# Kernel tuning notes

Measured on AMD Instinct MI355X. Metric: run time of the kernel, lower is better.

The kernel has to match this reference:

```python
import jax, jax.numpy as jnp
import numpy as np

B, T, I, H, V, E = 512, 256, 256, 1024, 1024, 8
FUT = 64


def _lstm_cell(x_t, h, c, Wih, Whh, b):
    # PyTorch gate order: i, f, g, o. b = b_ih + b_hh (mathematically identical).
    z = x_t @ Wih.T + h @ Whh.T + b  # [B, 4H]
    i, f, g, o = jnp.split(z, 4, axis=-1)
    i = jax.nn.sigmoid(i)
    f = jax.nn.sigmoid(f)
    g = jnp.tanh(g)
    o = jax.nn.sigmoid(o)
    c_new = f * c + i * g
    h_new = o * jnp.tanh(c_new)
    return h_new, c_new


def setup_inputs() -> dict:
    key = jax.random.key(0)
    ks = jax.random.split(key, 10)
    s = 0.02
    return {
        "x_hist": jax.random.normal(ks[0], (B, T, I), jnp.float32),
        "enc_Wih": jax.random.normal(ks[1], (4 * H, I), jnp.float32) * s,
        "enc_Whh": jax.random.normal(ks[2], (4 * H, H), jnp.float32) * s,
        "enc_b": jnp.zeros((4 * H,), jnp.float32),
        "embed_W": jax.random.normal(ks[3], (V, E), jnp.float32),
        "dec_Wih": jax.random.normal(ks[4], (4 * H, E), jnp.float32) * s,
        "dec_Whh": jax.random.normal(ks[5], (4 * H, H), jnp.float32) * s,
        "dec_b": jnp.zeros((4 * H,), jnp.float32),
        "fc_W": jax.random.normal(ks[6], (V, H), jnp.float32) * s,
        "fc_b": jnp.zeros((V,), jnp.float32),
        "future_len": FUT,
    }


def reference(x_hist, enc_Wih, enc_Whh, enc_b, embed_W, dec_Wih, dec_Whh,
              dec_b, fc_W, fc_b, future_len):
    bsz = x_hist.shape[0]
    h0 = jnp.zeros((bsz, enc_Whh.shape[1]), x_hist.dtype)
    c0 = jnp.zeros_like(h0)

    # Encoder LSTM over history (batch_first): scan over time.
    def enc_step(carry, x_t):
        h, c = carry
        h, c = _lstm_cell(x_t, h, c, enc_Wih, enc_Whh, enc_b)
        return (h, c), None

    (h, c), _ = jax.lax.scan(enc_step, (h0, c0), jnp.swapaxes(x_hist, 0, 1))

    y0 = jnp.zeros((bsz,), jnp.int32)

    def dec_step(carry, _):
        h, c, y_prev = carry
        x = embed_W[y_prev]                       # [B, E] embedding lookup
        h, c = _lstm_cell(x, h, c, dec_Wih, dec_Whh, dec_b)
        logits = h @ fc_W.T + fc_b                # [B, V]
        y = jnp.argmax(logits, axis=1).astype(jnp.int32)
        return (h, c, y), logits

    _, logits = jax.lax.scan(dec_step, (h, c, y0), None, length=future_len)
    return jnp.swapaxes(logits, 0, 1)             # [B, future_len, V]
```

## Files before the change

kernel.cpp:

```cpp
#include <hip/hip_runtime.h>
#include <cmath>

typedef __attribute__((ext_vector_type(8))) short short8;
typedef __attribute__((ext_vector_type(4))) float f32x4;

#define B_SZ 512
#define T_SZ 256
#define I_SZ 256
#define H_SZ 1024
#define V_SZ 1024
#define E_SZ 8
#define FUT 64

#define KVE 3840
#define KVD 3200
#define KVF 3072
#define APE 2560
#define APD 2176

static __device__ __forceinline__ ushort f2bf(float v) {
    uint32_t u = __float_as_uint(v);
    uint32_t r = (u + 0x7fffu + ((u >> 16) & 1u)) >> 16;
    return (ushort)r;
}
static __device__ __forceinline__ float bf2f(ushort b) {
    return __uint_as_float(((uint32_t)b) << 16);
}
static __device__ __forceinline__ uint32_t fmono(float f) {
    uint32_t u = __float_as_uint(f);
    return (u & 0x80000000u) ? ~u : (u | 0x80000000u);
}
template<int N>
static __device__ __forceinline__ void waitvm() {
    if constexpr (N == 0)      asm volatile("s_waitcnt vmcnt(0)" ::: "memory");
    else if constexpr (N == 2) asm volatile("s_waitcnt vmcnt(2)" ::: "memory");
    else if constexpr (N == 3) asm volatile("s_waitcnt vmcnt(3)" ::: "memory");
    else if constexpr (N == 4) asm volatile("s_waitcnt vmcnt(4)" ::: "memory");
    else if constexpr (N == 6) asm volatile("s_waitcnt vmcnt(6)" ::: "memory");
}

#define GLD16(gp, lp)                                                          \
    __builtin_amdgcn_global_load_lds(                                         \
        (const __attribute__((address_space(1))) void*)(gp),                  \
        (__attribute__((address_space(3))) void*)(lp), 16, 0, 0)

template<int MFR, int NFR, int NTPX,
         int NKP, int PT1, int PO0, int PO1,
         int NKS, int ST1, int SO0, int SO1, bool GATES>
__global__ __launch_bounds__(256) void gemm_step(
    const ushort* __restrict__ A, int astr,
    const ushort* __restrict__ W, int kv,
    const float* __restrict__ bias,
    float* __restrict__ c,
    ushort* __restrict__ hdest, int ldh,
    const float* __restrict__ xsrc, ushort* __restrict__ xdest,
    float* __restrict__ out, int ldo,
    unsigned long long* __restrict__ keys)
{
    constexpr int ABUF = MFR * 2048;
    constexpr int WBUF = NFR * 4096;
    __shared__ __align__(16) ushort lds[3 * ABUF + 3 * WBUF];

    const int tid = threadIdx.x;
    const int lane = tid & 63;
    const int wid = tid >> 6;
    const int wm = wid >> 1, wn = wid & 1;
    const int l15 = lane & 15, lq = lane >> 4;
    const int l7 = lane & 7, l3 = lane >> 3;

    const int flat = blockIdx.x;
    const int xcd = flat & 7, slot = flat >> 3;
    const int n_tile = xcd * NTPX + (slot % NTPX);
    const int m_tile = slot / NTPX;
    const int m0 = m_tile * (MFR * 32);
    const int n0 = n_tile * (NFR * 32);

    f32x4 acc[MFR][NFR];
#pragma unroll
    for (int m = 0; m < MFR; ++m)
#pragma unroll
        for (int n = 0; n < NFR; ++n) { f32x4 z = {0.f, 0.f, 0.f, 0.f}; acc[m][n] = z; }

    auto stageA = [&](int kcA, int bufi) {
        ushort* ab = &lds[bufi * ABUF];
#pragma unroll
        for (int i = 0; i < MFR; ++i) {
            const int rowg = (i * 4 + wid) * 8;
            const int row = rowg + l3;
            GLD16(A + (size_t)(m0 + row) * astr + kcA + ((l7 ^ (row & 7)) * 8),
                  ab + rowg * 64);
        }
    };
    auto stageP = [&](int p, int bufi) {
        stageA(p * 64 + (p < PT1 ? PO0 : PO1), bufi);
        const int kcW = p * 128;
        ushort* wb = &lds[3 * ABUF + bufi * WBUF];
#pragma unroll
        for (int i = 0; i < 2 * NFR; ++i) {
            const int rowg = (i * 4 + wid) * 4;
            const int row = rowg + lq;
            GLD16(W + (size_t)(n0 + row) * kv + kcW + ((l15 ^ (row & 15)) * 8),
                  wb + rowg * 128);
        }
    };
    auto stageS = [&](int s, int bufi) {
        stageA(s * 64 + (s < ST1 ? SO0 : SO1), bufi);
        const int kcW = NKP * 128 + s * 64;
        ushort* wb = &lds[3 * ABUF + bufi * WBUF];
#pragma unroll
        for (int i = 0; i < NFR; ++i) {
            const int rowg = (i * 4 + wid) * 8;
            const int row = rowg + l3;
            GLD16(W + (size_t)(n0 + row) * kv + kcW + ((l7 ^ (row & 7)) * 8),
                  wb + rowg * 64);
        }
    };
    auto compP = [&](int bufi) {
        const ushort* ab = &lds[bufi * ABUF];
        const ushort* wb = &lds[3 * ABUF + bufi * WBUF];
#pragma unroll
        for (int kk = 0; kk < 2; ++kk) {
            short8 af[MFR];
#pragma unroll
            for (int m = 0; m < MFR; ++m) {
                const int row = wm * (MFR * 16) + m * 16 + l15;
                af[m] = *(const short8*)
                    &ab[row * 64 + (((kk * 4 + lq) ^ (row & 7)) * 8)];
            }
#pragma unroll
            for (int sub = 0; sub < 2; ++sub) {
                short8 wf[NFR];
#pragma unroll
                for (int n = 0; n < NFR; ++n) {
                    const int row = wn * (NFR * 16) + n * 16 + l15;
                    wf[n] = *(const short8*)
                        &wb[row * 128 + (((sub * 8 + kk * 4 + lq) ^ (row & 15)) * 8)];
                }
#pragma unroll
                for (int m = 0; m < MFR; ++m)
#pragma unroll
                    for (int n = 0; n < NFR; ++n)
                        acc[m][n] = __builtin_amdgcn_mfma_f32_16x16x32_bf16(
                            af[m], wf[n], acc[m][n], 0, 0, 0);
            }
        }
    };
    auto compS = [&](int bufi) {
        const ushort* ab = &lds[bufi * ABUF];
        const ushort* wb = &lds[3 * ABUF + bufi * WBUF];
#pragma unroll
        for (int kk = 0; kk < 2; ++kk) {
            short8 af[MFR], wf[NFR];
#pragma unroll
            for (int m = 0; m < MFR; ++m) {
                const int row = wm * (MFR * 16) + m * 16 + l15;
                af[m] = *(const short8*)
                    &ab[row * 64 + (((kk * 4 + lq) ^ (row & 7)) * 8)];
            }
#pragma unroll
            for (int n = 0; n < NFR; ++n) {
                const int row = wn * (NFR * 16) + n * 16 + l15;
                wf[n] = *(const short8*)
                    &wb[row * 64 + (((kk * 4 + lq) ^ (row & 7)) * 8)];
            }
#pragma unroll
            for (int m = 0; m < MFR; ++m)
#pragma unroll
                for (int n = 0; n < NFR; ++n)
                    acc[m][n] = __builtin_amdgcn_mfma_f32_16x16x32_bf16(
                        af[m], wf[n], acc[m][n], 0, 0, 0);
        }
    };

    auto STG = [&](int i, int b) { if (i < NKP) stageP(i, b); else stageS(i - NKP, b); };

    constexpr int NT = NKP + NKS;
    constexpr int GP = MFR + 2 * NFR;
    constexpr int GS = MFR + NFR;

    STG(0, 0);
    STG(1, 1);
#pragma unroll 1
    for (int i0 = 0; i0 < NT; i0 += 3) {
#pragma unroll
        for (int j = 0; j < 3; ++j) {
            const int i = i0 + j;
            if (i < NT) {
                if (i + 1 < NKP)     waitvm<GP>();
                else if (i + 1 < NT) waitvm<GS>();
                else                 waitvm<0>();
                __builtin_amdgcn_s_barrier();
                if (i + 2 < NT) STG(i + 2, (j + 2) % 3);
                if (i < NKP) compP(j); else compS(j);
            }
        }
    }

    if constexpr (GATES) {
        float* zs = (float*)&lds[0];
        __syncthreads();
#pragma unroll
        for (int m = 0; m < MFR; ++m)
#pragma unroll
            for (int n = 0; n < NFR; ++n)
#pragma unroll
                for (int r = 0; r < 4; ++r)
                    zs[(wm * 32 + m * 16 + lq * 4 + r) * 65 +
                       wn * 32 + n * 16 + l15] = acc[m][n][r];
        __syncthreads();

        const int row = tid & 63;
        const int jl0 = (tid >> 6) * 4;
        const int grow = m0 + row;
        const int jg = n_tile * 16 + jl0;
        const f32x4 bi4 = *(const f32x4*)&bias[n0 + jl0];
        const f32x4 bf4 = *(const f32x4*)&bias[n0 + 16 + jl0];
        const f32x4 bg4 = *(const f32x4*)&bias[n0 + 32 + jl0];
        const f32x4 bo4 = *(const f32x4*)&bias[n0 + 48 + jl0];
        f32x4 cv = *(f32x4*)&c[(size_t)grow * H_SZ + jg];
        ushort hh[4], hl[4];
#pragma unroll
        for (int jj = 0; jj < 4; ++jj) {
            const float zi = zs[row * 65 + jl0 + jj] + bi4[jj];
            const float zf = zs[row * 65 + 16 + jl0 + jj] + bf4[jj];
            const float zg = zs[row * 65 + 32 + jl0 + jj] + bg4[jj];
            const float zo = zs[row * 65 + 48 + jl0 + jj] + bo4[jj];
            const float ig = 1.f / (1.f + expf(-zi));
            const float fg = 1.f / (1.f + expf(-zf));
            const float gg = tanhf(zg);
            const float og = 1.f / (1.f + expf(-zo));
            const float cn = fg * cv[jj] + ig * gg;
            cv[jj] = cn;
            const float hv = og * tanhf(cn);
            hh[jj] = f2bf(hv);
            hl[jj] = f2bf(hv - bf2f(hh[jj]));
        }
        *(f32x4*)&c[(size_t)grow * H_SZ + jg] = cv;
        ushort* hd = hdest + (size_t)grow * ldh + jg;
        uint hv2[2], lv2[2];
        hv2[0] = (uint)hh[0] | ((uint)hh[1] << 16);
        hv2[1] = (uint)hh[2] | ((uint)hh[3] << 16);
        lv2[0] = (uint)hl[0] | ((uint)hl[1] << 16);
        lv2[1] = (uint)hl[2] | ((uint)hl[3] << 16);
        *(uint*)&hd[0] = hv2[0];
        *(uint*)&hd[2] = hv2[1];
        *(uint*)&hd[1024] = lv2[0];
        *(uint*)&hd[1026] = lv2[1];

        if (xdest) {
            const int idx = flat * 256 + tid;
            const int b = idx >> 8, i = idx & 255;
            const float v = xsrc[(size_t)b * (T_SZ * I_SZ) + i];
            const ushort hi = f2bf(v), lo = f2bf(v - bf2f(hi));
            xdest[(size_t)b * APE + i] = hi;
            xdest[(size_t)b * APE + 256 + i] = lo;
        }
    } else {
        float vals[4];
        const int col = n0 + wn * 16 + l15;
        const float bv = bias[col];
#pragma unroll
        for (int r = 0; r < 4; ++r) {
            const int row = m0 + wm * 16 + lq * 4 + r;
            vals[r] = acc[0][0][r] + bv;
            out[(size_t)row * ldo + col] = vals[r];
        }
        if (keys) {
            float* zs = (float*)&lds[0];
            __syncthreads();
#pragma unroll
            for (int r = 0; r < 4; ++r)
                zs[(wm * 16 + lq * 4 + r) * 33 + wn * 16 + l15] = vals[r];
            __syncthreads();
            if (tid < 32) {
                const int row = tid;
                float best = zs[row * 33];
                int bc = 0;
#pragma unroll
                for (int cc = 1; cc < 32; ++cc) {
                    const float x = zs[row * 33 + cc];
                    if (x > best) { best = x; bc = cc; }
                }
                const unsigned long long key =
                    ((unsigned long long)fmono(best) << 32) |
                    (unsigned long long)(V_SZ - 1 - (n0 + bc));
                atomicMax(&keys[m0 + row], key);
            }
        }
    }
}

__global__ __launch_bounds__(256) void gather_embed(
    unsigned long long* __restrict__ keys,
    const float* __restrict__ embed_W,
    ushort* __restrict__ xdest)
{
    const int idx = blockIdx.x * 256 + threadIdx.x;
    const int b = idx >> 3, e = idx & 7;
    const unsigned long long key = keys[b];
    const int yb = V_SZ - 1 - (int)(key & 0xffffffffu);
    const float v = embed_W[(size_t)yb * E_SZ + e];
    const ushort hi = f2bf(v), lo = f2bf(v - bf2f(hi));
    ushort* xd = xdest + (size_t)b * APD;
    xd[e] = hi;
    xd[8 + e] = hi;
    xd[16 + e] = lo;
    if (e == 0) keys[b] = 0ull;
}

__global__ void pack_enc(const float* __restrict__ Wih, const float* __restrict__ Whh,
                         const float* __restrict__ b, ushort* __restrict__ Wp,
                         float* __restrict__ bp)
{
    const int k = blockIdx.x * 256 + threadIdx.x;
    const int np = blockIdx.y;
    const int orig = ((np >> 4) & 3) * H_SZ + (np >> 6) * 16 + (np & 15);
    float v; bool lo = false;
    if (k < 2560) {
        const int p = k >> 7, cc = k & 63;
        lo = (k >> 6) & 1;
        v = (p < 4) ? Wih[(size_t)orig * I_SZ + p * 64 + cc]
                    : Whh[(size_t)orig * H_SZ + (p - 4) * 64 + cc];
    } else {
        const int s = (k - 2560) >> 6, cc = k & 63;
        v = (s < 4) ? Wih[(size_t)orig * I_SZ + s * 64 + cc]
                    : Whh[(size_t)orig * H_SZ + (s - 4) * 64 + cc];
    }
    const ushort hi = f2bf(v);
    Wp[(size_t)np * KVE + k] = lo ? f2bf(v - bf2f(hi)) : hi;
    if (k == 0) bp[np] = b[orig];
}

__global__ void pack_dec(const float* __restrict__ Wih, const float* __restrict__ Whh,
                         const float* __restrict__ b, ushort* __restrict__ Wp,
                         float* __restrict__ bp)
{
    const int k = blockIdx.x * 256 + threadIdx.x;
    const int np = blockIdx.y;
    if (k >= KVD) return;
    const int orig = ((np >> 4) & 3) * H_SZ + (np >> 6) * 16 + (np & 15);
    float v = 0.f; bool lo = false; bool zero = false;
    if (k < 2048) {
        const int p = k >> 7, cc = k & 63;
        lo = (k >> 6) & 1;
        v = Whh[(size_t)orig * H_SZ + p * 64 + cc];
    } else {
        const int s = (k - 2048) >> 6, cc = k & 63;
        if (s < 2) {
            const int j = s * 64 + cc;
            if (j < 8)       v = Wih[(size_t)orig * E_SZ + j];
            else if (j < 16) { v = Wih[(size_t)orig * E_SZ + j - 8]; lo = true; }
            else if (j < 24) v = Wih[(size_t)orig * E_SZ + j - 16];
            else             zero = true;
        } else {
            v = Whh[(size_t)orig * H_SZ + (s - 2) * 64 + cc];
        }
    }
    ushort w = 0;
    if (!zero) { const ushort hi = f2bf(v); w = lo ? f2bf(v - bf2f(hi)) : hi; }
    Wp[(size_t)np * KVD + k] = w;
    if (k == 0) bp[np] = b[orig];
}

__global__ void pack_fc(const float* __restrict__ W, ushort* __restrict__ Wp)
{
    const int k = blockIdx.x * 256 + threadIdx.x;
    const int np = blockIdx.y;
    float v; bool lo = false;
    if (k < 2048) {
        const int p = k >> 7, cc = k & 63;
        lo = (k >> 6) & 1;
        v = W[(size_t)np * H_SZ + p * 64 + cc];
    } else {
        const int s = (k - 2048) >> 6, cc = k & 63;
        v = W[(size_t)np * H_SZ + s * 64 + cc];
    }
    const ushort hi = f2bf(v);
    Wp[(size_t)np * KVF + k] = lo ? f2bf(v - bf2f(hi)) : hi;
}

__global__ void init_all(const float* __restrict__ x0,
                         const float* __restrict__ embed_W,
                         float* __restrict__ c,
                         ushort* __restrict__ Aenc0,
                         ushort* __restrict__ Adec0,
                         ushort* __restrict__ Adec1,
                         unsigned long long* __restrict__ keys)
{
    const int idx = blockIdx.x * 256 + threadIdx.x;
    {
        const int b = idx >> 11, k = idx & 2047;
        Aenc0[(size_t)b * APE + 512 + k] = 0;
    }
    if (idx < B_SZ * H_SZ) c[idx] = 0.f;
    if (idx < B_SZ) keys[idx] = 0ull;
    if (idx < B_SZ * I_SZ) {
        const int b = idx >> 8, i = idx & 255;
        const float v = x0[(size_t)b * (T_SZ * I_SZ) + i];
        const ushort hi = f2bf(v), lo = f2bf(v - bf2f(hi));
        Aenc0[(size_t)b * APE + i] = hi;
        Aenc0[(size_t)b * APE + 256 + i] = lo;
    }
    if (idx < B_SZ * 104) {
        const int b = idx / 104, col = 24 + idx % 104;
        Adec0[(size_t)b * APD + col] = 0;
        Adec1[(size_t)b * APD + col] = 0;
    }
    if (idx < B_SZ * 24) {
        const int b = idx / 24, col = idx % 24;
        float v;
        if (col < 8)       v = embed_W[col];
        else if (col < 16) v = embed_W[col - 8];
        else               v = embed_W[col - 16];
        const ushort hi = f2bf(v);
        Adec0[(size_t)b * APD + col] = (col < 16) ? hi : f2bf(v - bf2f(hi));
    }
}

extern "C" void kernel_launch(void* const* d_in, const int* in_sizes, int n_in,
                              void* d_out, int out_size, void* d_ws, size_t ws_size,
                              hipStream_t stream)
{
    const float* x_hist  = (const float*)d_in[0];
    const float* enc_Wih = (const float*)d_in[1];
    const float* enc_Whh = (const float*)d_in[2];
    const float* enc_b   = (const float*)d_in[3];
    const float* embed_W = (const float*)d_in[4];
    const float* dec_Wih = (const float*)d_in[5];
    const float* dec_Whh = (const float*)d_in[6];
    const float* dec_b   = (const float*)d_in[7];
    const float* fc_W    = (const float*)d_in[8];
    const float* fc_b    = (const float*)d_in[9];
    float* out = (float*)d_out;

    char* p = (char*)d_ws;
    auto alloc = [&](size_t bytes) {
        char* r = p;
        p += (bytes + 255) & ~(size_t)255;
        return r;
    };
    ushort* W_enc  = (ushort*)alloc((size_t)4096 * KVE * 2);
    ushort* W_dec  = (ushort*)alloc((size_t)4096 * KVD * 2);
    ushort* W_fc   = (ushort*)alloc((size_t)1024 * KVF * 2);
    ushort* A_enc0 = (ushort*)alloc((size_t)B_SZ * APE * 2);
    ushort* A_enc1 = (ushort*)alloc((size_t)B_SZ * APE * 2);
    ushort* A_dec0 = (ushort*)alloc((size_t)B_SZ * APD * 2);
    ushort* A_dec1 = (ushort*)alloc((size_t)B_SZ * APD * 2);
    float*  cbuf   = (float*)alloc((size_t)B_SZ * H_SZ * 4);
    float*  bpe    = (float*)alloc(4096 * 4);
    float*  bpd    = (float*)alloc(4096 * 4);
    unsigned long long* keys = (unsigned long long*)alloc(B_SZ * 8);

    const dim3 blk(256);
    hipLaunchKernelGGL(pack_enc, dim3(15, 4096), blk, 0, stream, enc_Wih, enc_Whh, enc_b, W_enc, bpe);
    hipLaunchKernelGGL(pack_dec, dim3(13, 4096), blk, 0, stream, dec_Wih, dec_Whh, dec_b, W_dec, bpd);
    hipLaunchKernelGGL(pack_fc,  dim3(12, 1024), blk, 0, stream, fc_W, W_fc);
    hipLaunchKernelGGL(init_all, dim3(4096), blk, 0, stream, x_hist, embed_W, cbuf, A_enc0, A_dec0, A_dec1, keys);

    ushort* Ae[2] = {A_enc0, A_enc1};
    ushort* Ad[2] = {A_dec0, A_dec1};

    for (int t = 0; t < T_SZ; ++t) {
        ushort* hdst; int ldh; const float* xs; ushort* xd;
        if (t < T_SZ - 1) {
            hdst = Ae[(t + 1) & 1] + 512; ldh = APE;
            xs = x_hist + (size_t)(t + 1) * I_SZ;
            xd = Ae[(t + 1) & 1];
        } else {
            hdst = Ad[0] + 128; ldh = APD;
            xs = nullptr; xd = nullptr;
        }
        hipLaunchKernelGGL((gemm_step<2, 2, 8, 20, 4, 0, 256, 20, 4, 256, 1280, true>),
                           dim3(512), blk, 0, stream,
                           Ae[t & 1], APE, W_enc, KVE, bpe, cbuf,
                           hdst, ldh, xs, xd, (float*)nullptr, 0,
                           (unsigned long long*)nullptr);
    }

    for (int t = 0; t < FUT; ++t) {
        hipLaunchKernelGGL((gemm_step<2, 2, 8, 16, 16, 128, 128, 18, 2, 0, 1024, true>),
                           dim3(512), blk, 0, stream,
                           Ad[t & 1], APD, W_dec, KVD, bpd, cbuf,
                           Ad[(t + 1) & 1] + 128, APD,
                           (const float*)nullptr, (ushort*)nullptr,
                           (float*)nullptr, 0,
                           (unsigned long long*)nullptr);
        float* logits = out + (size_t)t * V_SZ;
        hipLaunchKernelGGL((gemm_step<1, 1, 4, 16, 16, 128, 128, 16, 16, 1152, 1152, false>),
                           dim3(512), blk, 0, stream,
                           Ad[(t + 1) & 1], APD, W_fc, KVF, fc_b,
                           (float*)nullptr, (ushort*)nullptr, 0,
                           (const float*)nullptr, (ushort*)nullptr,
                           logits, FUT * V_SZ, keys);
        hipLaunchKernelGGL(gather_embed, dim3(16), blk, 0, stream,
                           keys, embed_W, Ad[(t + 1) & 1]);
    }
}
```

Baseline: 9.829 ms.

## Store activations in MFMA fragment-tiled layout and load A directly to registers

Activation matrices (x, h hi/lo, embeddings) are now written in a fragment-native tiled layout of 16-row by 32-column tiles, so each lane can load its MFMA A operand straight from global memory into registers. This removes A staging through LDS and the LDS reads that fed it, which shrinks shared memory to weight buffers only. All producers (the gates epilogue, init_all, gather_embed) are rewritten to scatter into the new layout. In exchange, A fragments are held in registers across a three-deep prefetch ring, which raises register pressure, and the direct global loads may coalesce less well than the previous LDS path.

```diff
diff --git a/kernel.cpp b/kernel.cpp
--- a/kernel.cpp
+++ b/kernel.cpp
@@ -37,6 +37,7 @@
     else if constexpr (N == 3) asm volatile("s_waitcnt vmcnt(3)" ::: "memory");
     else if constexpr (N == 4) asm volatile("s_waitcnt vmcnt(4)" ::: "memory");
     else if constexpr (N == 6) asm volatile("s_waitcnt vmcnt(6)" ::: "memory");
+    else if constexpr (N == 8) asm volatile("s_waitcnt vmcnt(8)" ::: "memory");
 }
 
 #define GLD16(gp, lp)                                                          \
@@ -52,14 +53,13 @@
     const ushort* __restrict__ W, int kv,
     const float* __restrict__ bias,
     float* __restrict__ c,
-    ushort* __restrict__ hdest, int ldh,
+    ushort* __restrict__ hdest, int hoff, int hkt,
     const float* __restrict__ xsrc, ushort* __restrict__ xdest,
     float* __restrict__ out, int ldo,
     unsigned long long* __restrict__ keys)
 {
-    constexpr int ABUF = MFR * 2048;
     constexpr int WBUF = NFR * 4096;
-    __shared__ __align__(16) ushort lds[3 * ABUF + 3 * WBUF];
+    __shared__ __align__(16) ushort lds[3 * WBUF];
 
     const int tid = threadIdx.x;
     const int lane = tid & 63;
@@ -74,6 +74,7 @@
     const int m_tile = slot / NTPX;
     const int m0 = m_tile * (MFR * 32);
     const int n0 = n_tile * (NFR * 32);
+    const int KT = astr >> 5;
 
     f32x4 acc[MFR][NFR];
 #pragma unroll
@@ -81,20 +82,9 @@
 #pragma unroll
         for (int n = 0; n < NFR; ++n) { f32x4 z = {0.f, 0.f, 0.f, 0.f}; acc[m][n] = z; }
 
-    auto stageA = [&](int kcA, int bufi) {
-        ushort* ab = &lds[bufi * ABUF];
-#pragma unroll
-        for (int i = 0; i < MFR; ++i) {
-            const int rowg = (i * 4 + wid) * 8;
-            const int row = rowg + l3;
-            GLD16(A + (size_t)(m0 + row) * astr + kcA + ((l7 ^ (row & 7)) * 8),
-                  ab + rowg * 64);
-        }
-    };
-    auto stageP = [&](int p, int bufi) {
-        stageA(p * 64 + (p < PT1 ? PO0 : PO1), bufi);
+    auto stageWP = [&](int p, int bufi) {
         const int kcW = p * 128;
-        ushort* wb = &lds[3 * ABUF + bufi * WBUF];
+        ushort* wb = &lds[bufi * WBUF];
 #pragma unroll
         for (int i = 0; i < 2 * NFR; ++i) {
             const int rowg = (i * 4 + wid) * 4;
@@ -103,10 +93,9 @@
                   wb + rowg * 128);
         }
     };
-    auto stageS = [&](int s, int bufi) {
-        stageA(s * 64 + (s < ST1 ? SO0 : SO1), bufi);
+    auto stageWS = [&](int s, int bufi) {
         const int kcW = NKP * 128 + s * 64;
-        ushort* wb = &lds[3 * ABUF + bufi * WBUF];
+        ushort* wb = &lds[bufi * WBUF];
 #pragma unroll
         for (int i = 0; i < NFR; ++i) {
             const int rowg = (i * 4 + wid) * 8;
@@ -115,18 +104,24 @@
                   wb + rowg * 64);
         }
     };
-    auto compP = [&](int bufi) {
-        const ushort* ab = &lds[bufi * ABUF];
-        const ushort* wb = &lds[3 * ABUF + bufi * WBUF];
+    auto AFL = [&](int i, short8 (&dst)[MFR][2]) {
+        int kcA;
+        if (i < NKP) kcA = i * 64 + (i < PT1 ? PO0 : PO1);
+        else { const int s = i - NKP; kcA = s * 64 + (s < ST1 ? SO0 : SO1); }
+        const int ktb = kcA >> 5;
+#pragma unroll
+        for (int m = 0; m < MFR; ++m) {
+            const int rt = (m0 + wm * (MFR * 16) + m * 16) >> 4;
+#pragma unroll
+            for (int kk = 0; kk < 2; ++kk)
+                dst[m][kk] = *(const short8*)
+                    &A[(((size_t)rt * KT + ktb + kk) * 64 + lane) * 8];
+        }
+    };
+    auto compP = [&](int bufi, const short8 (&af)[MFR][2]) {
+        const ushort* wb = &lds[bufi * WBUF];
 #pragma unroll
         for (int kk = 0; kk < 2; ++kk) {
-            short8 af[MFR];
-#pragma unroll
-            for (int m = 0; m < MFR; ++m) {
-                const int row = wm * (MFR * 16) + m * 16 + l15;
-                af[m] = *(const short8*)
-                    &ab[row * 64 + (((kk * 4 + lq) ^ (row & 7)) * 8)];
-            }
 #pragma unroll
             for (int sub = 0; sub < 2; ++sub) {
                 short8 wf[NFR];
@@ -141,22 +136,15 @@
 #pragma unroll
                     for (int n = 0; n < NFR; ++n)
                         acc[m][n] = __builtin_amdgcn_mfma_f32_16x16x32_bf16(
-                            af[m], wf[n], acc[m][n], 0, 0, 0);
+                            af[m][kk], wf[n], acc[m][n], 0, 0, 0);
             }
         }
     };
-    auto compS = [&](int bufi) {
-        const ushort* ab = &lds[bufi * ABUF];
-        const ushort* wb = &lds[3 * ABUF + bufi * WBUF];
+    auto compS = [&](int bufi, const short8 (&af)[MFR][2]) {
+        const ushort* wb = &lds[bufi * WBUF];
 #pragma unroll
         for (int kk = 0; kk < 2; ++kk) {
-            short8 af[MFR], wf[NFR];
-#pragma unroll
-            for (int m = 0; m < MFR; ++m) {
-                const int row = wm * (MFR * 16) + m * 16 + l15;
-                af[m] = *(const short8*)
-                    &ab[row * 64 + (((kk * 4 + lq) ^ (row & 7)) * 8)];
-            }
+            short8 wf[NFR];
 #pragma unroll
             for (int n = 0; n < NFR; ++n) {
                 const int row = wn * (NFR * 16) + n * 16 + l15;
@@ -168,30 +156,29 @@
 #pragma unroll
                 for (int n = 0; n < NFR; ++n)
                     acc[m][n] = __builtin_amdgcn_mfma_f32_16x16x32_bf16(
-                        af[m], wf[n], acc[m][n], 0, 0, 0);
+                        af[m][kk], wf[n], acc[m][n], 0, 0, 0);
         }
     };
 
-    auto STG = [&](int i, int b) { if (i < NKP) stageP(i, b); else stageS(i - NKP, b); };
+    auto STGW = [&](int i, int b) { if (i < NKP) stageWP(i, b); else stageWS(i - NKP, b); };
 
     constexpr int NT = NKP + NKS;
-    constexpr int GP = MFR + 2 * NFR;
-    constexpr int GS = MFR + NFR;
-
-    STG(0, 0);
-    STG(1, 1);
+
+    short8 afs[3][MFR][2];
+    STGW(0, 0); AFL(0, afs[0]);
+    STGW(1, 1); AFL(1, afs[1]);
 #pragma unroll 1
     for (int i0 = 0; i0 < NT; i0 += 3) {
 #pragma unroll
         for (int j = 0; j < 3; ++j) {
             const int i = i0 + j;
             if (i < NT) {
-                if (i + 1 < NKP)     waitvm<GP>();
-                else if (i + 1 < NT) waitvm<GS>();
+                if (i + 1 < NKP)     waitvm<2 * NFR + 2 * MFR>();
+                else if (i + 1 < NT) waitvm<NFR + 2 * MFR>();
                 else                 waitvm<0>();
                 __builtin_amdgcn_s_barrier();
-                if (i + 2 < NT) STG(i + 2, (j + 2) % 3);
-                if (i < NKP) compP(j); else compS(j);
+                if (i + 2 < NT) { STGW(i + 2, (j + 2) % 3); AFL(i + 2, afs[(j + 2) % 3]); }
+                if (i < NKP) compP(j, afs[j]); else compS(j, afs[j]);
             }
         }
     }
@@ -236,24 +223,30 @@
             hl[jj] = f2bf(hv - bf2f(hh[jj]));
         }
         *(f32x4*)&c[(size_t)grow * H_SZ + jg] = cv;
-        ushort* hd = hdest + (size_t)grow * ldh + jg;
+        const int colh = hoff + jg;
+        const int rt = grow >> 4;
+        const int lh = (grow & 15) + (((colh >> 3) & 3) << 4);
+        const size_t hb = (((size_t)rt * hkt + (colh >> 5)) * 64 + lh) * 8 + (colh & 7);
         uint hv2[2], lv2[2];
         hv2[0] = (uint)hh[0] | ((uint)hh[1] << 16);
         hv2[1] = (uint)hh[2] | ((uint)hh[3] << 16);
         lv2[0] = (uint)hl[0] | ((uint)hl[1] << 16);
         lv2[1] = (uint)hl[2] | ((uint)hl[3] << 16);
-        *(uint*)&hd[0] = hv2[0];
-        *(uint*)&hd[2] = hv2[1];
-        *(uint*)&hd[1024] = lv2[0];
-        *(uint*)&hd[1026] = lv2[1];
+        *(uint*)&hdest[hb]         = hv2[0];
+        *(uint*)&hdest[hb + 2]     = hv2[1];
+        *(uint*)&hdest[hb + 16384] = lv2[0];
+        *(uint*)&hdest[hb + 16386] = lv2[1];
 
         if (xdest) {
             const int idx = flat * 256 + tid;
             const int b = idx >> 8, i = idx & 255;
             const float v = xsrc[(size_t)b * (T_SZ * I_SZ) + i];
             const ushort hi = f2bf(v), lo = f2bf(v - bf2f(hi));
-            xdest[(size_t)b * APE + i] = hi;
-            xdest[(size_t)b * APE + 256 + i] = lo;
+            const int rtx = b >> 4;
+            const int lx = (b & 15) + (((i >> 3) & 3) << 4);
+            const int e = i & 7;
+            xdest[(((size_t)rtx * 80 + (i >> 5)) * 64 + lx) * 8 + e] = hi;
+            xdest[(((size_t)rtx * 80 + 8 + (i >> 5)) * 64 + lx) * 8 + e] = lo;
         }
     } else {
         float vals[4];
@@ -301,10 +294,11 @@
     const int yb = V_SZ - 1 - (int)(key & 0xffffffffu);
     const float v = embed_W[(size_t)yb * E_SZ + e];
     const ushort hi = f2bf(v), lo = f2bf(v - bf2f(hi));
-    ushort* xd = xdest + (size_t)b * APD;
-    xd[e] = hi;
-    xd[8 + e] = hi;
-    xd[16 + e] = lo;
+    const size_t base = (size_t)(b >> 4) * 68 * 512;
+    const int l0 = b & 15;
+    xdest[base + (size_t)(l0)      * 8 + e] = hi;
+    xdest[base + (size_t)(l0 + 16) * 8 + e] = hi;
+    xdest[base + (size_t)(l0 + 32) * 8 + e] = lo;
     if (e == 0) keys[b] = 0ull;
 }
 
@@ -389,22 +383,32 @@
 {
     const int idx = blockIdx.x * 256 + threadIdx.x;
     {
-        const int b = idx >> 11, k = idx & 2047;
-        Aenc0[(size_t)b * APE + 512 + k] = 0;
-    }
-    if (idx < B_SZ * H_SZ) c[idx] = 0.f;
-    if (idx < B_SZ) keys[idx] = 0ull;
-    if (idx < B_SZ * I_SZ) {
+        f32x4 z = {0.f, 0.f, 0.f, 0.f};
+        *(f32x4*)&c[(size_t)idx * 4] = z;
+    }
+    {
+        const int b = idx >> 8, g = idx & 255;
+        const int col = 512 + g * 8;
+        const int l = (b & 15) + (((col >> 3) & 3) << 4);
+        short8 z8 = {};
+        *(short8*)&Aenc0[(((size_t)(b >> 4) * 80 + (col >> 5)) * 64 + l) * 8] = z8;
+    }
+    {
         const int b = idx >> 8, i = idx & 255;
         const float v = x0[(size_t)b * (T_SZ * I_SZ) + i];
         const ushort hi = f2bf(v), lo = f2bf(v - bf2f(hi));
-        Aenc0[(size_t)b * APE + i] = hi;
-        Aenc0[(size_t)b * APE + 256 + i] = lo;
-    }
+        const int l = (b & 15) + (((i >> 3) & 3) << 4);
+        const int e = i & 7;
+        Aenc0[(((size_t)(b >> 4) * 80 + (i >> 5)) * 64 + l) * 8 + e] = hi;
+        Aenc0[(((size_t)(b >> 4) * 80 + 8 + (i >> 5)) * 64 + l) * 8 + e] = lo;
+    }
+    if (idx < B_SZ) keys[idx] = 0ull;
     if (idx < B_SZ * 104) {
         const int b = idx / 104, col = 24 + idx % 104;
-        Adec0[(size_t)b * APD + col] = 0;
-        Adec1[(size_t)b * APD + col] = 0;
+        const int l = (b & 15) + (((col >> 3) & 3) << 4);
+        const size_t o = (((size_t)(b >> 4) * 68 + (col >> 5)) * 64 + l) * 8 + (col & 7);
+        Adec0[o] = 0;
+        Adec1[o] = 0;
     }
     if (idx < B_SZ * 24) {
         const int b = idx / 24, col = idx % 24;
@@ -413,7 +417,9 @@
         else if (col < 16) v = embed_W[col - 8];
         else               v = embed_W[col - 16];
         const ushort hi = f2bf(v);
-        Adec0[(size_t)b * APD + col] = (col < 16) ? hi : f2bf(v - bf2f(hi));
+        const ushort w = (col < 16) ? hi : f2bf(v - bf2f(hi));
+        const int l = (b & 15) + ((col >> 3) << 4);
+        Adec0[((size_t)(b >> 4) * 68 * 64 + l) * 8 + (col & 7)] = w;
     }
 }
 
@@ -455,25 +461,25 @@
     hipLaunchKernelGGL(pack_enc, dim3(15, 4096), blk, 0, stream, enc_Wih, enc_Whh, enc_b, W_enc, bpe);
     hipLaunchKernelGGL(pack_dec, dim3(13, 4096), blk, 0, stream, dec_Wih, dec_Whh, dec_b, W_dec, bpd);
     hipLaunchKernelGGL(pack_fc,  dim3(12, 1024), blk, 0, stream, fc_W, W_fc);
-    hipLaunchKernelGGL(init_all, dim3(4096), blk, 0, stream, x_hist, embed_W, cbuf, A_enc0, A_dec0, A_dec1, keys);
+    hipLaunchKernelGGL(init_all, dim3(512), blk, 0, stream, x_hist, embed_W, cbuf, A_enc0, A_dec0, A_dec1, keys);
 
     ushort* Ae[2] = {A_enc0, A_enc1};
     ushort* Ad[2] = {A_dec0, A_dec1};
 
     for (int t = 0; t < T_SZ; ++t) {
-        ushort* hdst; int ldh; const float* xs; ushort* xd;
+        ushort* hdst; int hoff, hkt; const float* xs; ushort* xd;
         if (t < T_SZ - 1) {
-            hdst = Ae[(t + 1) & 1] + 512; ldh = APE;
+            hdst = Ae[(t + 1) & 1]; hoff = 512; hkt = 80;
             xs = x_hist + (size_t)(t + 1) * I_SZ;
             xd = Ae[(t + 1) & 1];
         } else {
-            hdst = Ad[0] + 128; ldh = APD;
+            hdst = Ad[0]; hoff = 128; hkt = 68;
             xs = nullptr; xd = nullptr;
         }
         hipLaunchKernelGGL((gemm_step<2, 2, 8, 20, 4, 0, 256, 20, 4, 256, 1280, true>),
                            dim3(512), blk, 0, stream,
                            Ae[t & 1], APE, W_enc, KVE, bpe, cbuf,
-                           hdst, ldh, xs, xd, (float*)nullptr, 0,
+                           hdst, hoff, hkt, xs, xd, (float*)nullptr, 0,
                            (unsigned long long*)nullptr);
     }
 
@@ -481,7 +487,7 @@
         hipLaunchKernelGGL((gemm_step<2, 2, 8, 16, 16, 128, 128, 18, 2, 0, 1024, true>),
                            dim3(512), blk, 0, stream,
                            Ad[t & 1], APD, W_dec, KVD, bpd, cbuf,
-                           Ad[(t + 1) & 1] + 128, APD,
+                           Ad[(t + 1) & 1], 128, 68,
                            (const float*)nullptr, (ushort*)nullptr,
                            (float*)nullptr, 0,
                            (unsigned long long*)nullptr);
@@ -489,7 +495,7 @@
         hipLaunchKernelGGL((gemm_step<1, 1, 4, 16, 16, 128, 128, 16, 16, 1152, 1152, false>),
                            dim3(512), blk, 0, stream,
                            Ad[(t + 1) & 1], APD, W_fc, KVF, fc_b,
-                           (float*)nullptr, (ushort*)nullptr, 0,
+                           (float*)nullptr, (ushort*)nullptr, 0, 0,
                            (const float*)nullptr, (ushort*)nullptr,
                            logits, FUT * V_SZ, keys);
         hipLaunchKernelGGL(gather_embed, dim3(16), blk, 0, stream,
```

Result: slower. 15.10 ms (+53.7%).

## Fuse embedding gather into decoder gate GEMM with triple-buffered argmax keys

Applied to the files above, without the earlier changes.

Removes the separate gather_embed launch per decode step. The decoder gate kernel now reads the previous step's argmax keys, gathers the embedding rows and writes them into its own A buffer before staging. It also zeroes the key buffer that the next FC step will use. Keys rotate through three buffers so the reads, the zeroing and the atomicMax writes do not conflict. This saves 64 small launches, but it risks a race: the A columns are written by each block and then loaded by the same block via global_load_lds with no visible fence, and other blocks also read those rows.

```diff
diff --git a/kernel.cpp b/kernel.cpp
--- a/kernel.cpp
+++ b/kernel.cpp
@@ -46,7 +46,7 @@
 
 template<int MFR, int NFR, int NTPX,
          int NKP, int PT1, int PO0, int PO1,
-         int NKS, int ST1, int SO0, int SO1, bool GATES>
+         int NKS, int ST1, int SO0, int SO1, bool GATES, bool DECXC>
 __global__ __launch_bounds__(256) void gemm_step(
     const ushort* __restrict__ A, int astr,
     const ushort* __restrict__ W, int kv,
@@ -55,7 +55,10 @@
     ushort* __restrict__ hdest, int ldh,
     const float* __restrict__ xsrc, ushort* __restrict__ xdest,
     float* __restrict__ out, int ldo,
-    unsigned long long* __restrict__ keys)
+    unsigned long long* __restrict__ keys,
+    const unsigned long long* __restrict__ kread,
+    unsigned long long* __restrict__ kzero,
+    const float* __restrict__ embW)
 {
     constexpr int ABUF = MFR * 2048;
     constexpr int WBUF = NFR * 4096;
@@ -74,6 +77,26 @@
     const int m_tile = slot / NTPX;
     const int m0 = m_tile * (MFR * 32);
     const int n0 = n_tile * (NFR * 32);
+
+    if constexpr (DECXC) {
+        if (tid < 192) {
+            const int row = tid & 63, trip = tid >> 6;
+            const int grow = m0 + row;
+            const int yb = V_SZ - 1 - (int)(kread[grow] & 0xffffffffu);
+            short8 v8;
+#pragma unroll
+            for (int e = 0; e < 8; ++e) {
+                const float v = embW[(size_t)yb * E_SZ + e];
+                const ushort hi = f2bf(v);
+                v8[e] = (short)(trip < 2 ? hi : f2bf(v - bf2f(hi)));
+            }
+            *(short8*)&xdest[(size_t)grow * astr + trip * 8] = v8;
+        }
+        if (flat == 0) {
+            kzero[tid] = 0ull;
+            kzero[tid + 256] = 0ull;
+        }
+    }
 
     f32x4 acc[MFR][NFR];
 #pragma unroll
@@ -247,13 +270,15 @@
         *(uint*)&hd[1024] = lv2[0];
         *(uint*)&hd[1026] = lv2[1];
 
-        if (xdest) {
-            const int idx = flat * 256 + tid;
-            const int b = idx >> 8, i = idx & 255;
-            const float v = xsrc[(size_t)b * (T_SZ * I_SZ) + i];
-            const ushort hi = f2bf(v), lo = f2bf(v - bf2f(hi));
-            xdest[(size_t)b * APE + i] = hi;
-            xdest[(size_t)b * APE + 256 + i] = lo;
+        if constexpr (!DECXC) {
+            if (xdest) {
+                const int idx = flat * 256 + tid;
+                const int b = idx >> 8, i = idx & 255;
+                const float v = xsrc[(size_t)b * (T_SZ * I_SZ) + i];
+                const ushort hi = f2bf(v), lo = f2bf(v - bf2f(hi));
+                xdest[(size_t)b * APE + i] = hi;
+                xdest[(size_t)b * APE + 256 + i] = lo;
+            }
         }
     } else {
         float vals[4];
@@ -288,24 +313,6 @@
             }
         }
     }
-}
-
-__global__ __launch_bounds__(256) void gather_embed(
-    unsigned long long* __restrict__ keys,
-    const float* __restrict__ embed_W,
-    ushort* __restrict__ xdest)
-{
-    const int idx = blockIdx.x * 256 + threadIdx.x;
-    const int b = idx >> 3, e = idx & 7;
-    const unsigned long long key = keys[b];
-    const int yb = V_SZ - 1 - (int)(key & 0xffffffffu);
-    const float v = embed_W[(size_t)yb * E_SZ + e];
-    const ushort hi = f2bf(v), lo = f2bf(v - bf2f(hi));
-    ushort* xd = xdest + (size_t)b * APD;
-    xd[e] = hi;
-    xd[8 + e] = hi;
-    xd[16 + e] = lo;
-    if (e == 0) keys[b] = 0ull;
 }
 
 __global__ void pack_enc(const float* __restrict__ Wih, const float* __restrict__ Whh,
@@ -380,12 +387,11 @@
 }
 
 __global__ void init_all(const float* __restrict__ x0,
-                         const float* __restrict__ embed_W,
                          float* __restrict__ c,
                          ushort* __restrict__ Aenc0,
                          ushort* __restrict__ Adec0,
                          ushort* __restrict__ Adec1,
-                         unsigned long long* __restrict__ keys)
+                         unsigned long long* __restrict__ kb)
 {
     const int idx = blockIdx.x * 256 + threadIdx.x;
     {
@@ -393,7 +399,11 @@
         Aenc0[(size_t)b * APE + 512 + k] = 0;
     }
     if (idx < B_SZ * H_SZ) c[idx] = 0.f;
-    if (idx < B_SZ) keys[idx] = 0ull;
+    if (idx < B_SZ) {
+        kb[idx] = 0ull;
+        kb[512 + idx] = 0ull;
+        kb[1024 + idx] = 1023ull;
+    }
     if (idx < B_SZ * I_SZ) {
         const int b = idx >> 8, i = idx & 255;
         const float v = x0[(size_t)b * (T_SZ * I_SZ) + i];
@@ -405,15 +415,6 @@
         const int b = idx / 104, col = 24 + idx % 104;
         Adec0[(size_t)b * APD + col] = 0;
         Adec1[(size_t)b * APD + col] = 0;
-    }
-    if (idx < B_SZ * 24) {
-        const int b = idx / 24, col = idx % 24;
-        float v;
-        if (col < 8)       v = embed_W[col];
-        else if (col < 16) v = embed_W[col - 8];
-        else               v = embed_W[col - 16];
-        const ushort hi = f2bf(v);
-        Adec0[(size_t)b * APD + col] = (col < 16) ? hi : f2bf(v - bf2f(hi));
     }
 }
 
@@ -449,16 +450,17 @@
     float*  cbuf   = (float*)alloc((size_t)B_SZ * H_SZ * 4);
     float*  bpe    = (float*)alloc(4096 * 4);
     float*  bpd    = (float*)alloc(4096 * 4);
-    unsigned long long* keys = (unsigned long long*)alloc(B_SZ * 8);
+    unsigned long long* kb = (unsigned long long*)alloc(3 * B_SZ * 8);
 
     const dim3 blk(256);
     hipLaunchKernelGGL(pack_enc, dim3(15, 4096), blk, 0, stream, enc_Wih, enc_Whh, enc_b, W_enc, bpe);
     hipLaunchKernelGGL(pack_dec, dim3(13, 4096), blk, 0, stream, dec_Wih, dec_Whh, dec_b, W_dec, bpd);
     hipLaunchKernelGGL(pack_fc,  dim3(12, 1024), blk, 0, stream, fc_W, W_fc);
-    hipLaunchKernelGGL(init_all, dim3(4096), blk, 0, stream, x_hist, embed_W, cbuf, A_enc0, A_dec0, A_dec1, keys);
+    hipLaunchKernelGGL(init_all, dim3(4096), blk, 0, stream, x_hist, cbuf, A_enc0, A_dec0, A_dec1, kb);
 
     ushort* Ae[2] = {A_enc0, A_enc1};
     ushort* Ad[2] = {A_dec0, A_dec1};
+    unsigned long long* knull = nullptr;
 
     for (int t = 0; t < T_SZ; ++t) {
         ushort* hdst; int ldh; const float* xs; ushort* xd;
@@ -470,29 +472,34 @@
             hdst = Ad[0] + 128; ldh = APD;
             xs = nullptr; xd = nullptr;
         }
-        hipLaunchKernelGGL((gemm_step<2, 2, 8, 20, 4, 0, 256, 20, 4, 256, 1280, true>),
+        hipLaunchKernelGGL((gemm_step<2, 2, 8, 20, 4, 0, 256, 20, 4, 256, 1280, true, false>),
                            dim3(512), blk, 0, stream,
                            Ae[t & 1], APE, W_enc, KVE, bpe, cbuf,
                            hdst, ldh, xs, xd, (float*)nullptr, 0,
-                           (unsigned long long*)nullptr);
+                           knull, (const unsigned long long*)nullptr, knull,
+                           (const float*)nullptr);
     }
 
     for (int t = 0; t < FUT; ++t) {
-        hipLaunchKernelGGL((gemm_step<2, 2, 8, 16, 16, 128, 128, 18, 2, 0, 1024, true>),
+        hipLaunchKernelGGL((gemm_step<2, 2, 8, 16, 16, 128, 128, 18, 2, 0, 1024, true, true>),
                            dim3(512), blk, 0, stream,
                            Ad[t & 1], APD, W_dec, KVD, bpd, cbuf,
                            Ad[(t + 1) & 1] + 128, APD,
-                           (const float*)nullptr, (ushort*)nullptr,
+                           (const float*)nullptr, Ad[t & 1],
                            (float*)nullptr, 0,
-                           (unsigned long long*)nullptr);
+                           knull,
+                           kb + ((t + 2) % 3) * B_SZ,
+                           kb + ((t + 1) % 3) * B_SZ,
+                           embed_W);
         float* logits = out + (size_t)t * V_SZ;
-        hipLaunchKernelGGL((gemm_step<1, 1, 4, 16, 16, 128, 128, 16, 16, 1152, 1152, false>),
+        hipLaunchKernelGGL((gemm_step<1, 1, 4, 16, 16, 128, 128, 16, 16, 1152, 1152, false, false>),
                            dim3(512), blk, 0, stream,
                            Ad[(t + 1) & 1], APD, W_fc, KVF, fc_b,
                            (float*)nullptr, (ushort*)nullptr, 0,
                            (const float*)nullptr, (ushort*)nullptr,
-                           logits, FUT * V_SZ, keys);
-        hipLaunchKernelGGL(gather_embed, dim3(16), blk, 0, stream,
-                           keys, embed_W, Ad[(t + 1) & 1]);
-    }
-}
+                           logits, FUT * V_SZ,
+                           kb + (t % 3) * B_SZ,
+                           (const unsigned long long*)nullptr, knull,
+                           (const float*)nullptr);
+    }
+}
```

After: 9.755 ms. No clear change (-0.7%).
